# Kernel optimization log

Measured on AMD Instinct MI355X. Metric: run time of the kernel, lower is better.

The kernel has to match this reference:

```python
import jax, jax.numpy as jnp
import numpy as np

SEQ, BATCH, D_MODEL = 128, 64, 2048
D_STATE, D_CONV, CHUNK = 16, 4, 32
D_INNER = int(1.2 * D_MODEL)      # 2457
GROUPS = 7                        # largest g<=8 dividing 2457
DT_RANK = max(4, D_MODEL // 64)   # 32
WIN = 8
NEG = -1e30


def setup_inputs() -> dict:
    key = jax.random.key(0)
    ks = jax.random.split(key, 8)
    w = lambda k, shape, s: (jax.random.normal(k, shape) * s).astype(jnp.float32)
    return {
        "x": jax.random.normal(ks[0], (SEQ, BATCH, D_MODEL), dtype=jnp.float32),
        "W_in": w(ks[1], (D_INNER, D_MODEL), 0.02),
        "b_in": jnp.zeros((D_INNER,), jnp.float32),
        "W_gate": w(ks[2], (D_INNER, D_MODEL), 0.02),
        "b_gate": jnp.zeros((D_INNER,), jnp.float32),
        "W_conv": w(ks[3], (D_INNER, D_INNER // GROUPS, D_CONV), 0.05),
        "b_conv": jnp.zeros((D_INNER,), jnp.float32),
        "W_xproj": w(ks[4], (DT_RANK + D_STATE, D_INNER), 0.02),
        "b_xproj": jnp.zeros((DT_RANK + D_STATE,), jnp.float32),
        "W_dt": w(ks[5], (D_INNER, DT_RANK), 0.1),
        "Dparam": jnp.full((D_INNER,), 0.1, jnp.float32),
        "W_out": w(ks[6], (D_MODEL, D_INNER), 0.02),
        "b_out": jnp.zeros((D_MODEL,), jnp.float32),
        "ln_w": jnp.ones((D_MODEL,), jnp.float32),
        "ln_b": jnp.zeros((D_MODEL,), jnp.float32),
    }


def reference(x, W_in, b_in, W_gate, b_gate, W_conv, b_conv,
              W_xproj, b_xproj, W_dt, Dparam, W_out, b_out, ln_w, ln_b):
    def process_chunk(xc_in):                      # [L, B, d_model]
        L = xc_in.shape[0]
        xi = xc_in @ W_in.T + b_in                 # [L, B, d_inner]
        z = xc_in @ W_gate.T + b_gate              # gate
        # causal grouped conv1d: torch pads both sides by d_conv-1 then
        # truncates [:L]  ==  left-pad (d_conv-1), VALID conv
        c = jnp.transpose(xi, (1, 2, 0))           # [B, d_inner, L]
        c = jnp.pad(c, ((0, 0), (0, 0), (D_CONV - 1, 0)))
        c = jax.lax.conv_general_dilated(
            c, W_conv, window_strides=(1,), padding='VALID',
            dimension_numbers=('NCH', 'OIH', 'NCH'),
            feature_group_count=GROUPS) + b_conv[None, :, None]
        xc = jax.nn.silu(jnp.transpose(c, (2, 0, 1)))   # [L, B, d_inner]
        # dt_t = softplus(dt_proj(x_proj(x_t)[:dt_rank])) + 1e-4
        xp = xc @ W_xproj.T + b_xproj
        dt = jax.nn.softplus(xp[..., :DT_RANK] @ W_dt.T) + 1e-4  # [L,B,d_inner]
        xpad = jnp.pad(xc, ((WIN - 1, 0), (0, 0), (0, 0)))
        windows = jnp.stack([xpad[k:k + L] for k in range(WIN)], axis=1)
        t = jnp.arange(L)
        kk = jnp.arange(WIN)
        offset = jnp.maximum(0, WIN - 1 - t)       # shift so arange starts at 0
        ar = kk[None, :] - offset[:, None]
        valid = ar >= 0
        logits = dt[:, None] * ar[:, :, None, None].astype(dt.dtype)
        logits = jnp.where(valid[:, :, None, None], logits, NEG)
        wgt = jax.nn.softmax(logits, axis=1)       # softmax over window
        local = jnp.sum(wgt * windows, axis=1)     # [L, B, d_inner]
        return (local + Dparam * xc) * jax.nn.sigmoid(z)

    # chunks are processed independently (window + conv restart per chunk)
    xr = x.reshape(SEQ // CHUNK, CHUNK, BATCH, D_MODEL)
    ys = jax.vmap(process_chunk)(xr).reshape(SEQ, BATCH, D_INNER)
    compressed = ys[-WIN:].mean(axis=0)            # mean of last 8 steps
    out = compressed @ W_out.T + b_out             # [B, d_model]
    mu = out.mean(-1, keepdims=True)
    var = ((out - mu) ** 2).mean(-1, keepdims=True)
    return ((out - mu) / jnp.sqrt(var + 1e-5)) * ln_w + ln_b
```

## Files before the change

### kernel.cpp

```cpp
#include <hip/hip_runtime.h>
#include <math.h>
#include <stdint.h>

#define DMODEL 2048
#define DINNER 2457
#define NI     2464
#define GROUPS 7
#define GCH    351
#define GP     352
#define GNP    384
#define NROW_XI 1152
#define NROW_Z  512
#define NCAT   5120
#define GATE0  2560
#define OUT_SPLITS 16
#define CONV_PLANE (GROUPS * GNP * GP)

typedef __attribute__((ext_vector_type(8))) __bf16 bf16x8;
typedef __attribute__((ext_vector_type(4))) float f32x4;
typedef __attribute__((ext_vector_type(8))) unsigned short ushort8;

__device__ inline unsigned short f2bf(float f) {
    union { float f; unsigned int u; } v; v.f = f;
    unsigned int u = v.u;
    return (unsigned short)((u + 0x7FFFu + ((u >> 16) & 1u)) >> 16);
}

__device__ inline int lds_addr(int row, int slot) {
    return row * 32 + ((slot ^ ((row >> 1) & 3)) << 3);
}

__device__ __forceinline__ void gload16(const unsigned short* g, unsigned short* l) {
    __builtin_amdgcn_global_load_lds(
        (const __attribute__((address_space(1))) unsigned int*)g,
        (__attribute__((address_space(3))) unsigned int*)l, 16, 0, 0);
}

#define CAST_B0 1152
#define CAST_B1 6066
#define CAST_B2 9435
__global__ __launch_bounds__(256)
void cast_all(const float* __restrict__ x110,
              const float* __restrict__ Win, const float* __restrict__ Wg,
              const float* __restrict__ Wc,
              unsigned short* __restrict__ A_x,
              unsigned short* __restrict__ B_cat,
              unsigned short* __restrict__ B_cv)
{
    int bx = blockIdx.x;
    if (bx < CAST_B0) {
        size_t t = (size_t)bx * 256 + threadIdx.x;
        const float4* s = (const float4*)x110 + t * 2;
        float4 a = s[0], b = s[1];
        ushort8 o;
        o[0]=f2bf(a.x); o[1]=f2bf(a.y); o[2]=f2bf(a.z); o[3]=f2bf(a.w);
        o[4]=f2bf(b.x); o[5]=f2bf(b.y); o[6]=f2bf(b.z); o[7]=f2bf(b.w);
        *(ushort8*)(A_x + t * 8) = o;
    } else if (bx < CAST_B1) {
        int idx = bx - CAST_B0;
        int half = idx >= DINNER;
        int cb = half ? idx - DINNER : idx;
        const float* src = half ? Wg : Win;
        size_t t = (size_t)cb * 256 + threadIdx.x;
        size_t elem = t * 8;
        size_t doff = elem + (half ? (size_t)GATE0 * DMODEL : 0);
        const float4* s = (const float4*)(src + elem);
        float4 a = s[0], b = s[1];
        ushort8 o;
        o[0]=f2bf(a.x); o[1]=f2bf(a.y); o[2]=f2bf(a.z); o[3]=f2bf(a.w);
        o[4]=f2bf(b.x); o[5]=f2bf(b.y); o[6]=f2bf(b.z); o[7]=f2bf(b.w);
        *(ushort8*)(B_cat + doff) = o;
    } else {
        int t = (bx - CAST_B1) * 256 + threadIdx.x;
        if (t >= DINNER * GCH) return;
        int oc = t / GCH, i = t - oc * GCH;
        float4 w = *(const float4*)(Wc + (size_t)t * 4);
        int g = oc / GCH, ol = oc - g * GCH;
        size_t base = (size_t)(g * GNP + ol) * GP + i;
        B_cv[0 * (size_t)CONV_PLANE + base] = f2bf(w.x);
        B_cv[1 * (size_t)CONV_PLANE + base] = f2bf(w.y);
        B_cv[2 * (size_t)CONV_PLANE + base] = f2bf(w.z);
        B_cv[3 * (size_t)CONV_PLANE + base] = f2bf(w.w);
        if (i == GCH - 1) {
            B_cv[0 * (size_t)CONV_PLANE + base + 1] = 0;
            B_cv[1 * (size_t)CONV_PLANE + base + 1] = 0;
            B_cv[2 * (size_t)CONV_PLANE + base + 1] = 0;
            B_cv[3 * (size_t)CONV_PLANE + base + 1] = 0;
        }
    }
}

#define NKF 64
__global__ __launch_bounds__(256)
void gemm_mfma_fused(const unsigned short* __restrict__ A,
                     const unsigned short* __restrict__ B,
                     const float* __restrict__ b_in,
                     const float* __restrict__ b_gate,
                     unsigned short* __restrict__ xi,
                     float* __restrict__ zb)
{
    __shared__ unsigned short sm[3 * 256 * 32];
    const int tid = threadIdx.x;
    const int w = tid >> 6, l = tid & 63;
    const int l15 = l & 15, l4 = l >> 4;
    const int wm = w >> 1, wn = w & 1;

    const int orig = blockIdx.x;
    const int xcd = orig & 7, lo = orig >> 3;
    const int logical = (xcd < 4 ? xcd * 33 : 132 + (xcd - 4) * 32) + lo;
    int mt, nt, is_gate;
    if (logical < 180) { nt = logical / 9; mt = logical % 9; is_gate = 0; }
    else { int b2 = logical - 180; nt = 20 + b2 / 4; mt = 5 + b2 % 4; is_gate = 1; }
    const int m0 = mt * 128, n0 = nt * 128;

    const int lr = l >> 2, slot = l & 3;
    const int r0 = w * 16 + lr, r1 = r0 + 64;
    const int xo0 = (slot ^ ((r0 >> 1) & 3)) << 3;
    const int xo1 = (slot ^ ((r1 >> 1) & 3)) << 3;
    const unsigned short* gA0 = A + (size_t)(m0 + r0) * DMODEL + xo0;
    const unsigned short* gA1 = A + (size_t)(m0 + r1) * DMODEL + xo1;
    const unsigned short* gB0 = B + (size_t)(n0 + r0) * DMODEL + xo0;
    const unsigned short* gB1 = B + (size_t)(n0 + r1) * DMODEL + xo1;
    unsigned short* dA0 = sm + w * 512;
    unsigned short* dA1 = sm + (w + 4) * 512;
    unsigned short* dB0 = sm + 4096 + w * 512;
    unsigned short* dB1 = sm + 4096 + (w + 4) * 512;

#define STAGE_G(buf, ks) do { int _o = (ks) * 32, _b = (buf) * 8192; \
    gload16(gA0 + _o, dA0 + _b); gload16(gA1 + _o, dA1 + _b); \
    gload16(gB0 + _o, dB0 + _b); gload16(gB1 + _o, dB1 + _b); } while (0)

    f32x4 acc[4][4] = {};
    auto compute = [&](const unsigned short* base) {
        bf16x8 af[4], bfr[4];
#pragma unroll
        for (int f = 0; f < 4; ++f)
            af[f] = *(const bf16x8*)(base + lds_addr(wm * 64 + f * 16 + l15, l4));
#pragma unroll
        for (int j = 0; j < 4; ++j)
            bfr[j] = *(const bf16x8*)(base + 4096 + lds_addr(wn * 64 + j * 16 + l15, l4));
#pragma unroll
        for (int i = 0; i < 4; ++i)
#pragma unroll
            for (int j = 0; j < 4; ++j)
                acc[i][j] = __builtin_amdgcn_mfma_f32_16x16x32_bf16(af[i], bfr[j], acc[i][j], 0, 0, 0);
    };

    STAGE_G(0, 0);
    STAGE_G(1, 1);
    int rbuf = 0, sbuf = 2;
    for (int ks = 0; ks < NKF - 1; ++ks) {
        asm volatile("s_waitcnt vmcnt(4)" ::: "memory");
        __builtin_amdgcn_s_barrier();
        if (ks < NKF - 2) STAGE_G(sbuf, ks + 2);
        compute(sm + rbuf * 8192);
        rbuf = rbuf == 2 ? 0 : rbuf + 1;
        sbuf = sbuf == 2 ? 0 : sbuf + 1;
    }
    asm volatile("s_waitcnt vmcnt(0)" ::: "memory");
    __builtin_amdgcn_s_barrier();
    compute(sm + rbuf * 8192);
#undef STAGE_G

    if (!is_gate) {
#pragma unroll
        for (int j = 0; j < 4; ++j) {
            int colg = n0 + wn * 64 + j * 16 + l15;
            if (colg < DINNER) {
                int g = colg / GCH, ci = colg - g * GCH;
                float bias = b_in[colg];
                size_t dco = (size_t)(g * GP + ci);
#pragma unroll
                for (int i = 0; i < 4; ++i)
#pragma unroll
                    for (int r = 0; r < 4; ++r) {
                        int row = m0 + wm * 64 + i * 16 + l4 * 4 + r;
                        xi[(size_t)row * NI + dco] = f2bf(acc[i][j][r] + bias);
                        if (ci == GCH - 1) xi[(size_t)row * NI + dco + 1] = 0;
                    }
            }
        }
    } else {
#pragma unroll
        for (int j = 0; j < 4; ++j) {
            int ng = n0 + wn * 64 + j * 16 + l15 - GATE0;
            if (ng < DINNER) {
                float bias = b_gate[ng];
#pragma unroll
                for (int i = 0; i < 4; ++i)
#pragma unroll
                    for (int r = 0; r < 4; ++r) {
                        int row = m0 + wm * 64 + i * 16 + l4 * 4 + r;
                        zb[(size_t)(row - 640) * NI + ng] = acc[i][j][r] + bias;
                    }
            }
        }
    }
}

#define NKC 44
__global__ __launch_bounds__(256)
void conv_mfma(const unsigned short* __restrict__ xi,
               const unsigned short* __restrict__ Bc,
               const float* __restrict__ bc,
               float* __restrict__ xcb)
{
    __shared__ unsigned short sm[3 * 192 * 32];
    const int tid = threadIdx.x;
    const int w = tid >> 6, l = tid & 63;
    const int l15 = l & 15, l4 = l >> 4;
    const int wm = w >> 1, wn = w & 1;

    const int orig = blockIdx.x;
    const int xcd = orig & 7, lo = orig >> 3;
    const int logical = (xcd < 3 ? xcd * 40 : 120 + (xcd - 3) * 39) + lo;
    const int gn = logical / 15, mt = logical % 15;
    const int g = gn / 3, nt = gn % 3;
    const int m0 = mt * 64;
    const int n0l = nt * 128;

    const int lr = l >> 2, slot = l & 3;
    const int rA = w * 16 + lr;
    const int rB0 = rA, rB1 = rA + 64;
    const int xoA  = (slot ^ ((rA  >> 1) & 3)) << 3;
    const int xoB1 = (slot ^ ((rB1 >> 1) & 3)) << 3;
    const unsigned short* gAb = xi + (size_t)(m0 + rA) * NI + g * GP + xoA;
    const unsigned short* gB0 = Bc + (size_t)(g * GNP + n0l + rB0) * GP + xoA;
    const unsigned short* gB1 = Bc + (size_t)(g * GNP + n0l + rB1) * GP + xoB1;
    unsigned short* dA  = sm + w * 512;
    unsigned short* dB0 = sm + 2048 + w * 512;
    unsigned short* dB1 = sm + 2048 + (w + 4) * 512;

#define STAGE_C(buf, ks) do { \
    int _tap = (ks) / 11, _kc = (ks) - _tap * 11, _b = (buf) * 6144; \
    size_t _ao = (size_t)(64 * _tap) * NI + _kc * 32; \
    size_t _bo = (size_t)_tap * CONV_PLANE + _kc * 32; \
    gload16(gAb + _ao, dA  + _b); \
    gload16(gB0 + _bo, dB0 + _b); \
    gload16(gB1 + _bo, dB1 + _b); } while (0)

    f32x4 acc[2][4] = {};
    auto compute = [&](const unsigned short* base) {
        bf16x8 af[2], bfr[4];
#pragma unroll
        for (int f = 0; f < 2; ++f)
            af[f] = *(const bf16x8*)(base + lds_addr(wm * 32 + f * 16 + l15, l4));
#pragma unroll
        for (int j = 0; j < 4; ++j)
            bfr[j] = *(const bf16x8*)(base + 2048 + lds_addr(wn * 64 + j * 16 + l15, l4));
#pragma unroll
        for (int i = 0; i < 2; ++i)
#pragma unroll
            for (int j = 0; j < 4; ++j)
                acc[i][j] = __builtin_amdgcn_mfma_f32_16x16x32_bf16(af[i], bfr[j], acc[i][j], 0, 0, 0);
    };

    STAGE_C(0, 0);
    STAGE_C(1, 1);
    int rbuf = 0, sbuf = 2;
    for (int ks = 0; ks < NKC - 1; ++ks) {
        asm volatile("s_waitcnt vmcnt(3)" ::: "memory");
        __builtin_amdgcn_s_barrier();
        if (ks < NKC - 2) STAGE_C(sbuf, ks + 2);
        compute(sm + rbuf * 6144);
        rbuf = rbuf == 2 ? 0 : rbuf + 1;
        sbuf = sbuf == 2 ? 0 : sbuf + 1;
    }
    asm volatile("s_waitcnt vmcnt(0)" ::: "memory");
    __builtin_amdgcn_s_barrier();
    compute(sm + rbuf * 6144);
#undef STAGE_C

#pragma unroll
    for (int j = 0; j < 4; ++j) {
        int ocl = n0l + wn * 64 + j * 16 + l15;
        if (ocl < GCH) {
            int ch = g * GCH + ocl;
            float bias = bc[ch];
#pragma unroll
            for (int i = 0; i < 2; ++i)
#pragma unroll
                for (int r = 0; r < 4; ++r) {
                    int row = m0 + wm * 32 + i * 16 + l4 * 4 + r;
                    float v = acc[i][j][r] + bias;
                    xcb[(size_t)row * NI + ch] = v / (1.f + expf(-v));
                }
        }
    }
}

__global__ __launch_bounds__(256)
void xproj_dt(const float* __restrict__ xc,
              const float* __restrict__ Wxp,
              const float* __restrict__ bxp,
              const float* __restrict__ Wdt,
              float* __restrict__ dtb)
{
    const int row = blockIdx.x;
    const float* a = xc + (size_t)(448 + row) * NI;
    float acc[32];
#pragma unroll
    for (int o = 0; o < 32; ++o) acc[o] = 0.f;
    for (int k = threadIdx.x; k < DINNER; k += 256) {
        float av = a[k];
#pragma unroll
        for (int o = 0; o < 32; ++o)
            acc[o] = fmaf(av, Wxp[(size_t)o * DINNER + k], acc[o]);
    }
#pragma unroll
    for (int o = 0; o < 32; ++o)
#pragma unroll
        for (int off = 32; off; off >>= 1)
            acc[o] += __shfl_down(acc[o], off);
    __shared__ float red[4][32];
    __shared__ float xp[32];
    const int wid = threadIdx.x >> 6, lane = threadIdx.x & 63;
    if (lane == 0)
#pragma unroll
        for (int o = 0; o < 32; ++o) red[wid][o] = acc[o];
    __syncthreads();
    if (threadIdx.x < 32) {
        int o = threadIdx.x;
        xp[o] = red[0][o] + red[1][o] + red[2][o] + red[3][o] + bxp[o];
    }
    __syncthreads();
    float xr[32];
#pragma unroll
    for (int k = 0; k < 32; ++k) xr[k] = xp[k];
    for (int o = threadIdx.x; o < DINNER; o += 256) {
        const float4* wp = (const float4*)(Wdt + (size_t)o * 32);
        float s = 0.f;
#pragma unroll
        for (int q = 0; q < 8; ++q) {
            float4 wv = wp[q];
            s = fmaf(xr[q * 4 + 0], wv.x, s);
            s = fmaf(xr[q * 4 + 1], wv.y, s);
            s = fmaf(xr[q * 4 + 2], wv.z, s);
            s = fmaf(xr[q * 4 + 3], wv.w, s);
        }
        float sp = fmaxf(s, 0.f) + log1pf(expf(-fabsf(s)));
        dtb[(size_t)row * NI + o] = sp + 1e-4f;
    }
}

__global__ __launch_bounds__(256)
void fuse_kernel(const float* __restrict__ xc, const float* __restrict__ z,
                 const float* __restrict__ dt, const float* __restrict__ Dp,
                 float* __restrict__ comp)
{
    const int d = blockIdx.x * 256 + threadIdx.x;
    const int b = blockIdx.y;
    if (d >= DINNER) return;
    float xcv[15];
#pragma unroll
    for (int tt = 0; tt < 15; ++tt) xcv[tt] = xc[(size_t)(tt * 64 + b) * NI + d];
    const float Dpd = Dp[d];
    float acc = 0.f;
#pragma unroll
    for (int s = 0; s < 8; ++s) {
        float dval = dt[(size_t)(s * 64 + b) * NI + d];
        float zval = z[(size_t)(s * 64 + b) * NI + d];
        float e = expf(-dval);
        float w = 1.f, wsum = 0.f, lsum = 0.f;
#pragma unroll
        for (int k = 7; k >= 0; --k) {
            wsum += w;
            lsum = fmaf(w, xcv[s + k], lsum);
            w *= e;
        }
        float local = lsum / wsum;
        float ys = (local + Dpd * xcv[s + 7]) / (1.f + expf(-zval));
        acc += ys;
    }
    comp[(size_t)b * NI + d] = acc * 0.125f;
}

__global__ __launch_bounds__(256)
void gemm_nt_splitk(const float* __restrict__ A, int lda,
                    const float* __restrict__ B, int ldb,
                    float* __restrict__ Cp, int ldc,
                    int M, int N, int K, int kchunk)
{
    __shared__ float As[16][68];
    __shared__ float Bs[16][68];
    const int tid = threadIdx.x;
    const int tx = tid & 15, ty = tid >> 4;
    const int m0 = blockIdx.y * 64, n0 = blockIdx.x * 64;
    const int kbeg = blockIdx.z * kchunk;
    const int kend = min(K, kbeg + kchunk);
    float* C = Cp + (size_t)blockIdx.z * M * ldc;
    float acc[4][4] = {};
    for (int k0 = kbeg; k0 < kend; k0 += 16) {
#pragma unroll
        for (int u = 0; u < 4; ++u) {
            int idx = u * 256 + tid;
            int r = idx >> 4, kk = idx & 15;
            int gk = k0 + kk;
            float av = 0.f, bv = 0.f;
            if (gk < kend) {
                av = A[(size_t)(m0 + r) * lda + gk];
                int nn = n0 + r;
                bv = (nn < N) ? B[(size_t)nn * ldb + gk] : 0.f;
            }
            As[kk][r] = av;
            Bs[kk][r] = bv;
        }
        __syncthreads();
#pragma unroll
        for (int kk = 0; kk < 16; ++kk) {
            float4 a4 = *(const float4*)&As[kk][ty * 4];
            float4 b4 = *(const float4*)&Bs[kk][tx * 4];
            float a[4] = {a4.x, a4.y, a4.z, a4.w};
            float b[4] = {b4.x, b4.y, b4.z, b4.w};
#pragma unroll
            for (int i = 0; i < 4; ++i)
#pragma unroll
                for (int j = 0; j < 4; ++j)
                    acc[i][j] = fmaf(a[i], b[j], acc[i][j]);
        }
        __syncthreads();
    }
#pragma unroll
    for (int i = 0; i < 4; ++i) {
        int m = m0 + ty * 4 + i;
#pragma unroll
        for (int j = 0; j < 4; ++j) {
            int n = n0 + tx * 4 + j;
            if (n < N) C[(size_t)m * ldc + n] = acc[i][j];
        }
    }
}

__global__ __launch_bounds__(256)
void ln_kernel(const float* __restrict__ Cp,
               const float* __restrict__ b_out,
               const float* __restrict__ lw, const float* __restrict__ lb,
               float* __restrict__ out)
{
    const int b = blockIdx.x;
    const int tid = threadIdx.x;
    __shared__ float red[4];
    float v[8];
    float s = 0.f;
#pragma unroll
    for (int i = 0; i < 8; ++i) {
        int col = i * 256 + tid;
        float acc = b_out[col];
#pragma unroll
        for (int p = 0; p < OUT_SPLITS; ++p)
            acc += Cp[(size_t)p * 64 * 2048 + b * 2048 + col];
        v[i] = acc; s += acc;
    }
#pragma unroll
    for (int off = 32; off; off >>= 1) s += __shfl_down(s, off);
    if ((tid & 63) == 0) red[tid >> 6] = s;
    __syncthreads();
    float mu = (red[0] + red[1] + red[2] + red[3]) / 2048.f;
    float s2 = 0.f;
#pragma unroll
    for (int i = 0; i < 8; ++i) { float dd = v[i] - mu; s2 += dd * dd; }
#pragma unroll
    for (int off = 32; off; off >>= 1) s2 += __shfl_down(s2, off);
    __syncthreads();
    if ((tid & 63) == 0) red[tid >> 6] = s2;
    __syncthreads();
    float var = (red[0] + red[1] + red[2] + red[3]) / 2048.f;
    float inv = rsqrtf(var + 1e-5f);
#pragma unroll
    for (int i = 0; i < 8; ++i) {
        int dcol = i * 256 + tid;
        out[b * 2048 + dcol] = (v[i] - mu) * inv * lw[dcol] + lb[dcol];
    }
}

extern "C" void kernel_launch(void* const* d_in, const int* in_sizes, int n_in,
                              void* d_out, int out_size, void* d_ws, size_t ws_size,
                              hipStream_t stream)
{
    const float* x      = (const float*)d_in[0];
    const float* W_in   = (const float*)d_in[1];
    const float* b_in   = (const float*)d_in[2];
    const float* W_gate = (const float*)d_in[3];
    const float* b_gate = (const float*)d_in[4];
    const float* W_conv = (const float*)d_in[5];
    const float* b_conv = (const float*)d_in[6];
    const float* W_xp   = (const float*)d_in[7];
    const float* b_xp   = (const float*)d_in[8];
    const float* W_dt   = (const float*)d_in[9];
    const float* Dp     = (const float*)d_in[10];
    const float* W_out  = (const float*)d_in[11];
    const float* b_out  = (const float*)d_in[12];
    const float* ln_w   = (const float*)d_in[13];
    const float* ln_b   = (const float*)d_in[14];
    float* out = (float*)d_out;

    float* ws = (float*)d_ws;
    auto alloc = [&](size_t nf) { float* p = ws; ws += (nf + 255) & ~(size_t)255; return p; };
    unsigned short* A_x   = (unsigned short*)alloc((size_t)NROW_XI * DMODEL / 2);
    unsigned short* B_cat = (unsigned short*)alloc((size_t)NCAT * DMODEL / 2);
    unsigned short* B_cv  = (unsigned short*)alloc((size_t)4 * CONV_PLANE / 2);
    unsigned short* xi_bf = (unsigned short*)alloc((size_t)NROW_XI * NI / 2);
    float* zb   = alloc((size_t)NROW_Z * NI);
    float* comp = alloc((size_t)64 * NI);
    float* xcb     = (float*)B_cat;
    float* outpart = (float*)B_cat + (size_t)960 * NI;
    float* dtb     = (float*)B_cv;

    cast_all<<<CAST_B2, 256, 0, stream>>>(x + (size_t)(110 * 64) * DMODEL,
                                          W_in, W_gate, W_conv, A_x, B_cat, B_cv);
    gemm_mfma_fused<<<260, 256, 0, stream>>>(A_x, B_cat, b_in, b_gate, xi_bf, zb);
    conv_mfma<<<315, 256, 0, stream>>>(xi_bf, B_cv, b_conv, xcb);
    xproj_dt<<<512, 256, 0, stream>>>(xcb, W_xp, b_xp, W_dt, dtb);
    {
        dim3 grid((DINNER + 255) / 256, 64);
        fuse_kernel<<<grid, 256, 0, stream>>>(xcb, zb, dtb, Dp, comp);
    }
    {
        const int kchunk = (DINNER + OUT_SPLITS - 1) / OUT_SPLITS;
        dim3 grid(DMODEL / 64, 1, OUT_SPLITS);
        gemm_nt_splitk<<<grid, 256, 0, stream>>>(comp, NI, W_out, DINNER,
                                                 outpart, DMODEL, 64, DMODEL, DINNER, kchunk);
    }
    ln_kernel<<<64, 256, 0, stream>>>(outpart, b_out, ln_w, ln_b, out);
}
```

Before: 135.9 us.

## Deepen GEMM/conv pipelines to 5 stages, add MFMA priority, batch xproj rows

Both MFMA kernels move from a 3-buffer LDS ring to a 5-buffer ring with 4 stages prefetched ahead, so more global loads are in flight while the tensor cores work. The drain is unrolled with explicit vmcnt waits. s_setprio raises wave priority around the MFMA block. xproj_dt now handles 4 rows per block, reusing each W_xproj and W_dt load across 4 rows and cutting the grid from 512 to 128 blocks. The cost is more LDS per block, which may lower occupancy, plus higher register pressure in xproj_dt from the 4x32 accumulator array.

```diff
diff --git a/kernel.cpp b/kernel.cpp
--- a/kernel.cpp
+++ b/kernel.cpp
@@ -99,7 +99,7 @@
                      unsigned short* __restrict__ xi,
                      float* __restrict__ zb)
 {
-    __shared__ unsigned short sm[3 * 256 * 32];
+    __shared__ unsigned short sm[5 * 256 * 32];
     const int tid = threadIdx.x;
     const int w = tid >> 6, l = tid & 63;
     const int l15 = l & 15, l4 = l >> 4;
@@ -139,24 +139,34 @@
 #pragma unroll
         for (int j = 0; j < 4; ++j)
             bfr[j] = *(const bf16x8*)(base + 4096 + lds_addr(wn * 64 + j * 16 + l15, l4));
+        __builtin_amdgcn_s_setprio(1);
 #pragma unroll
         for (int i = 0; i < 4; ++i)
 #pragma unroll
             for (int j = 0; j < 4; ++j)
                 acc[i][j] = __builtin_amdgcn_mfma_f32_16x16x32_bf16(af[i], bfr[j], acc[i][j], 0, 0, 0);
+        __builtin_amdgcn_s_setprio(0);
     };
 
-    STAGE_G(0, 0);
-    STAGE_G(1, 1);
-    int rbuf = 0, sbuf = 2;
-    for (int ks = 0; ks < NKF - 1; ++ks) {
-        asm volatile("s_waitcnt vmcnt(4)" ::: "memory");
+    STAGE_G(0, 0); STAGE_G(1, 1); STAGE_G(2, 2); STAGE_G(3, 3);
+    int rbuf = 0, sbuf = 4;
+    for (int ks = 0; ks < NKF - 4; ++ks) {
+        asm volatile("s_waitcnt vmcnt(12)" ::: "memory");
         __builtin_amdgcn_s_barrier();
-        if (ks < NKF - 2) STAGE_G(sbuf, ks + 2);
+        STAGE_G(sbuf, ks + 4);
         compute(sm + rbuf * 8192);
-        rbuf = rbuf == 2 ? 0 : rbuf + 1;
-        sbuf = sbuf == 2 ? 0 : sbuf + 1;
-    }
+        rbuf = rbuf == 4 ? 0 : rbuf + 1;
+        sbuf = sbuf == 4 ? 0 : sbuf + 1;
+    }
+    asm volatile("s_waitcnt vmcnt(12)" ::: "memory");
+    __builtin_amdgcn_s_barrier();
+    compute(sm + rbuf * 8192); rbuf = rbuf == 4 ? 0 : rbuf + 1;
+    asm volatile("s_waitcnt vmcnt(8)" ::: "memory");
+    __builtin_amdgcn_s_barrier();
+    compute(sm + rbuf * 8192); rbuf = rbuf == 4 ? 0 : rbuf + 1;
+    asm volatile("s_waitcnt vmcnt(4)" ::: "memory");
+    __builtin_amdgcn_s_barrier();
+    compute(sm + rbuf * 8192); rbuf = rbuf == 4 ? 0 : rbuf + 1;
     asm volatile("s_waitcnt vmcnt(0)" ::: "memory");
     __builtin_amdgcn_s_barrier();
     compute(sm + rbuf * 8192);
@@ -205,7 +215,7 @@
                const float* __restrict__ bc,
                float* __restrict__ xcb)
 {
-    __shared__ unsigned short sm[3 * 192 * 32];
+    __shared__ unsigned short sm[5 * 192 * 32];
     const int tid = threadIdx.x;
     const int w = tid >> 6, l = tid & 63;
     const int l15 = l & 15, l4 = l >> 4;
@@ -221,11 +231,11 @@
 
     const int lr = l >> 2, slot = l & 3;
     const int rA = w * 16 + lr;
-    const int rB0 = rA, rB1 = rA + 64;
+    const int rB1 = rA + 64;
     const int xoA  = (slot ^ ((rA  >> 1) & 3)) << 3;
     const int xoB1 = (slot ^ ((rB1 >> 1) & 3)) << 3;
     const unsigned short* gAb = xi + (size_t)(m0 + rA) * NI + g * GP + xoA;
-    const unsigned short* gB0 = Bc + (size_t)(g * GNP + n0l + rB0) * GP + xoA;
+    const unsigned short* gB0 = Bc + (size_t)(g * GNP + n0l + rA) * GP + xoA;
     const unsigned short* gB1 = Bc + (size_t)(g * GNP + n0l + rB1) * GP + xoB1;
     unsigned short* dA  = sm + w * 512;
     unsigned short* dB0 = sm + 2048 + w * 512;
@@ -248,24 +258,34 @@
 #pragma unroll
         for (int j = 0; j < 4; ++j)
             bfr[j] = *(const bf16x8*)(base + 2048 + lds_addr(wn * 64 + j * 16 + l15, l4));
+        __builtin_amdgcn_s_setprio(1);
 #pragma unroll
         for (int i = 0; i < 2; ++i)
 #pragma unroll
             for (int j = 0; j < 4; ++j)
                 acc[i][j] = __builtin_amdgcn_mfma_f32_16x16x32_bf16(af[i], bfr[j], acc[i][j], 0, 0, 0);
+        __builtin_amdgcn_s_setprio(0);
     };
 
-    STAGE_C(0, 0);
-    STAGE_C(1, 1);
-    int rbuf = 0, sbuf = 2;
-    for (int ks = 0; ks < NKC - 1; ++ks) {
-        asm volatile("s_waitcnt vmcnt(3)" ::: "memory");
+    STAGE_C(0, 0); STAGE_C(1, 1); STAGE_C(2, 2); STAGE_C(3, 3);
+    int rbuf = 0, sbuf = 4;
+    for (int ks = 0; ks < NKC - 4; ++ks) {
+        asm volatile("s_waitcnt vmcnt(9)" ::: "memory");
         __builtin_amdgcn_s_barrier();
-        if (ks < NKC - 2) STAGE_C(sbuf, ks + 2);
+        STAGE_C(sbuf, ks + 4);
         compute(sm + rbuf * 6144);
-        rbuf = rbuf == 2 ? 0 : rbuf + 1;
-        sbuf = sbuf == 2 ? 0 : sbuf + 1;
-    }
+        rbuf = rbuf == 4 ? 0 : rbuf + 1;
+        sbuf = sbuf == 4 ? 0 : sbuf + 1;
+    }
+    asm volatile("s_waitcnt vmcnt(9)" ::: "memory");
+    __builtin_amdgcn_s_barrier();
+    compute(sm + rbuf * 6144); rbuf = rbuf == 4 ? 0 : rbuf + 1;
+    asm volatile("s_waitcnt vmcnt(6)" ::: "memory");
+    __builtin_amdgcn_s_barrier();
+    compute(sm + rbuf * 6144); rbuf = rbuf == 4 ? 0 : rbuf + 1;
+    asm volatile("s_waitcnt vmcnt(3)" ::: "memory");
+    __builtin_amdgcn_s_barrier();
+    compute(sm + rbuf * 6144); rbuf = rbuf == 4 ? 0 : rbuf + 1;
     asm volatile("s_waitcnt vmcnt(0)" ::: "memory");
     __builtin_amdgcn_s_barrier();
     compute(sm + rbuf * 6144);
@@ -296,50 +316,69 @@
               const float* __restrict__ Wdt,
               float* __restrict__ dtb)
 {
-    const int row = blockIdx.x;
-    const float* a = xc + (size_t)(448 + row) * NI;
-    float acc[32];
-#pragma unroll
-    for (int o = 0; o < 32; ++o) acc[o] = 0.f;
+    const int r0 = blockIdx.x * 4;
+    const float* a = xc + (size_t)(448 + r0) * NI;
+    float acc[4][32];
+#pragma unroll
+    for (int ri = 0; ri < 4; ++ri)
+#pragma unroll
+        for (int o = 0; o < 32; ++o) acc[ri][o] = 0.f;
     for (int k = threadIdx.x; k < DINNER; k += 256) {
-        float av = a[k];
+        float av0 = a[k], av1 = a[NI + k], av2 = a[2 * NI + k], av3 = a[3 * NI + k];
+#pragma unroll
+        for (int o = 0; o < 32; ++o) {
+            float wv = Wxp[(size_t)o * DINNER + k];
+            acc[0][o] = fmaf(av0, wv, acc[0][o]);
+            acc[1][o] = fmaf(av1, wv, acc[1][o]);
+            acc[2][o] = fmaf(av2, wv, acc[2][o]);
+            acc[3][o] = fmaf(av3, wv, acc[3][o]);
+        }
+    }
+#pragma unroll
+    for (int ri = 0; ri < 4; ++ri)
 #pragma unroll
         for (int o = 0; o < 32; ++o)
-            acc[o] = fmaf(av, Wxp[(size_t)o * DINNER + k], acc[o]);
-    }
-#pragma unroll
-    for (int o = 0; o < 32; ++o)
-#pragma unroll
-        for (int off = 32; off; off >>= 1)
-            acc[o] += __shfl_down(acc[o], off);
-    __shared__ float red[4][32];
-    __shared__ float xp[32];
+#pragma unroll
+            for (int off = 32; off; off >>= 1)
+                acc[ri][o] += __shfl_down(acc[ri][o], off);
+    __shared__ float red[4][4][32];
+    __shared__ float xp[4][32];
     const int wid = threadIdx.x >> 6, lane = threadIdx.x & 63;
     if (lane == 0)
 #pragma unroll
-        for (int o = 0; o < 32; ++o) red[wid][o] = acc[o];
+        for (int ri = 0; ri < 4; ++ri)
+#pragma unroll
+            for (int o = 0; o < 32; ++o) red[wid][ri][o] = acc[ri][o];
     __syncthreads();
-    if (threadIdx.x < 32) {
-        int o = threadIdx.x;
-        xp[o] = red[0][o] + red[1][o] + red[2][o] + red[3][o] + bxp[o];
+    if (threadIdx.x < 128) {
+        int ri = threadIdx.x >> 5, o = threadIdx.x & 31;
+        xp[ri][o] = red[0][ri][o] + red[1][ri][o] + red[2][ri][o] + red[3][ri][o] + bxp[o];
     }
     __syncthreads();
-    float xr[32];
-#pragma unroll
-    for (int k = 0; k < 32; ++k) xr[k] = xp[k];
+    float xr[4][32];
+#pragma unroll
+    for (int ri = 0; ri < 4; ++ri)
+#pragma unroll
+        for (int k = 0; k < 32; ++k) xr[ri][k] = xp[ri][k];
     for (int o = threadIdx.x; o < DINNER; o += 256) {
         const float4* wp = (const float4*)(Wdt + (size_t)o * 32);
-        float s = 0.f;
+        float s0 = 0.f, s1 = 0.f, s2 = 0.f, s3 = 0.f;
 #pragma unroll
         for (int q = 0; q < 8; ++q) {
             float4 wv = wp[q];
-            s = fmaf(xr[q * 4 + 0], wv.x, s);
-            s = fmaf(xr[q * 4 + 1], wv.y, s);
-            s = fmaf(xr[q * 4 + 2], wv.z, s);
-            s = fmaf(xr[q * 4 + 3], wv.w, s);
-        }
-        float sp = fmaxf(s, 0.f) + log1pf(expf(-fabsf(s)));
-        dtb[(size_t)row * NI + o] = sp + 1e-4f;
+            s0 = fmaf(xr[0][q*4+0], wv.x, s0); s0 = fmaf(xr[0][q*4+1], wv.y, s0);
+            s0 = fmaf(xr[0][q*4+2], wv.z, s0); s0 = fmaf(xr[0][q*4+3], wv.w, s0);
+            s1 = fmaf(xr[1][q*4+0], wv.x, s1); s1 = fmaf(xr[1][q*4+1], wv.y, s1);
+            s1 = fmaf(xr[1][q*4+2], wv.z, s1); s1 = fmaf(xr[1][q*4+3], wv.w, s1);
+            s2 = fmaf(xr[2][q*4+0], wv.x, s2); s2 = fmaf(xr[2][q*4+1], wv.y, s2);
+            s2 = fmaf(xr[2][q*4+2], wv.z, s2); s2 = fmaf(xr[2][q*4+3], wv.w, s2);
+            s3 = fmaf(xr[3][q*4+0], wv.x, s3); s3 = fmaf(xr[3][q*4+1], wv.y, s3);
+            s3 = fmaf(xr[3][q*4+2], wv.z, s3); s3 = fmaf(xr[3][q*4+3], wv.w, s3);
+        }
+        dtb[(size_t)(r0 + 0) * NI + o] = fmaxf(s0, 0.f) + log1pf(expf(-fabsf(s0))) + 1e-4f;
+        dtb[(size_t)(r0 + 1) * NI + o] = fmaxf(s1, 0.f) + log1pf(expf(-fabsf(s1))) + 1e-4f;
+        dtb[(size_t)(r0 + 2) * NI + o] = fmaxf(s2, 0.f) + log1pf(expf(-fabsf(s2))) + 1e-4f;
+        dtb[(size_t)(r0 + 3) * NI + o] = fmaxf(s3, 0.f) + log1pf(expf(-fabsf(s3))) + 1e-4f;
     }
 }
 
@@ -510,7 +549,7 @@
                                           W_in, W_gate, W_conv, A_x, B_cat, B_cv);
     gemm_mfma_fused<<<260, 256, 0, stream>>>(A_x, B_cat, b_in, b_gate, xi_bf, zb);
     conv_mfma<<<315, 256, 0, stream>>>(xi_bf, B_cv, b_conv, xcb);
-    xproj_dt<<<512, 256, 0, stream>>>(xcb, W_xp, b_xp, W_dt, dtb);
+    xproj_dt<<<128, 256, 0, stream>>>(xcb, W_xp, b_xp, W_dt, dtb);
     {
         dim3 grid((DINNER + 255) / 256, 64);
         fuse_kernel<<<grid, 256, 0, stream>>>(xcb, zb, dtb, Dp, comp);
```

Result: slower. 140.7 us (+3.5%).
